# Kernel optimization log

Measured on AMD Instinct MI355X. Metric: run time of the kernel, lower is better.

The kernel has to match this reference:

```python
import jax, jax.numpy as jnp
import numpy as np

N_NODES = 100000

def gin_conv(x, edge_index, W, b):
    # PyG GINConv with eps=0: out = Linear(x + sum_{j->i} x_j)
    src, dst = edge_index[0], edge_index[1]
    agg = jax.ops.segment_sum(x[src], dst, num_segments=N_NODES)  # [N, d]
    return (x + agg) @ W + b

def setup_inputs() -> dict:
    key = jax.random.key(0)
    ks = jax.random.split(key, 8)
    x = jax.random.normal(ks[0], (N_NODES, 32), dtype=jnp.float32)
    edge_index = jax.random.randint(ks[1], (2, 1600000), 0, N_NODES, dtype=jnp.int64)
    def lin(k, fan_in, fan_out):
        kw, kb = jax.random.split(k)
        lim = 1.0 / np.sqrt(fan_in)
        W = jax.random.uniform(kw, (fan_in, fan_out), minval=-lim, maxval=lim, dtype=jnp.float32)
        b = jax.random.uniform(kb, (fan_out,), minval=-lim, maxval=lim, dtype=jnp.float32)
        return W, b
    W1, b1 = lin(ks[2], 32, 64)
    W2, b2 = lin(ks[3], 64, 64)
    W3, b3 = lin(ks[4], 64, 10)
    return {"x": x, "edge_index": edge_index,
            "W1": W1, "b1": b1, "W2": W2, "b2": b2, "W3": W3, "b3": b3}

def reference(x, edge_index, W1, b1, W2, b2, W3, b3):
    h = jax.nn.relu(gin_conv(x, edge_index, W1, b1))
    h = jax.nn.relu(gin_conv(h, edge_index, W2, b2))
    return gin_conv(h, edge_index, W3, b3)  # [N, classes] logits
```

## Files before the change

kernel.cpp:

```cpp
#include <hip/hip_runtime.h>


#define GIN_N 100000
#define NBUCKET 256
#define NB2 391
#define BSTRIDE 8192
#define EPT 16

typedef unsigned short bfu;
typedef float v2f __attribute__((ext_vector_type(2)));

__device__ __forceinline__ float bf_lo(unsigned int u) {
    return __uint_as_float(u << 16);
}
__device__ __forceinline__ float bf_hi(unsigned int u) {
    return __uint_as_float(u & 0xffff0000u);
}
__device__ __forceinline__ unsigned int f2bf(float f) {
    unsigned int u = __float_as_uint(f);
    return (u + 0x7fffu + ((u >> 16) & 1u)) >> 16;
}
__device__ __forceinline__ v2f fp8lo(unsigned u) {
    return __builtin_amdgcn_cvt_pk_f32_fp8(u, false);
}
__device__ __forceinline__ v2f fp8hi(unsigned u) {
    return __builtin_amdgcn_cvt_pk_f32_fp8(u, true);
}

template <int S>
__device__ __forceinline__ void blelloch_excl(int* a) {
#pragma unroll
    for (int d = 1; d < S; d <<= 1) {
        __syncthreads();
        int idx = (threadIdx.x + 1) * (d << 1) - 1;
        if (idx < S) a[idx] += a[idx - d];
    }
    __syncthreads();
    if (threadIdx.x == 0) a[S - 1] = 0;
#pragma unroll
    for (int d = S >> 1; d >= 1; d >>= 1) {
        __syncthreads();
        int idx = (threadIdx.x + 1) * (d << 1) - 1;
        if (idx < S) {
            int t = a[idx - d];
            a[idx - d] = a[idx];
            a[idx] += t;
        }
    }
    __syncthreads();
}

__global__ void f2q_kernel(const float* __restrict__ in,
                           unsigned* __restrict__ outq, int n8,
                           int* __restrict__ cursor) {
    int t = blockIdx.x * blockDim.x + threadIdx.x;
    if (blockIdx.x == 0) cursor[threadIdx.x] = 0;
    if (t >= n8) return;
    const float4* v = reinterpret_cast<const float4*>(in);
    float4 a = v[2 * t], b = v[2 * t + 1];
    unsigned w0 = 0, w1 = 0;
    w0 = __builtin_amdgcn_cvt_pk_fp8_f32(a.x, a.y, w0, false);
    w0 = __builtin_amdgcn_cvt_pk_fp8_f32(a.z, a.w, w0, true);
    w1 = __builtin_amdgcn_cvt_pk_fp8_f32(b.x, b.y, w1, false);
    w1 = __builtin_amdgcn_cvt_pk_fp8_f32(b.z, b.w, w1, true);
    reinterpret_cast<uint2*>(outq)[t] = make_uint2(w0, w1);
}

__global__ __launch_bounds__(256) void bucket_kernel(
        const int* __restrict__ src, const int* __restrict__ dst, int E,
        unsigned* __restrict__ bucketbuf, int* __restrict__ cursor) {
    __shared__ int h[NBUCKET];
    __shared__ int base[NBUCKET];
    int tid = threadIdx.x;
    int chunk0 = blockIdx.x * (256 * EPT);
    h[tid] = 0;
    __syncthreads();
    int myb[EPT];
    unsigned myrec[EPT];
#pragma unroll
    for (int i = 0; i < EPT; ++i) {
        int e = chunk0 + tid + i * 256;
        if (e < E) {
            int d = dst[e];
            int s = src[e];
            int b = d / NB2;
            myb[i] = b;
            myrec[i] = ((unsigned)(d - b * NB2) << 17) | (unsigned)s;
            atomicAdd(&h[b], 1);
        } else {
            myb[i] = -1;
        }
    }
    __syncthreads();
    base[tid] = atomicAdd(&cursor[tid], h[tid]);
    h[tid] = 0;
    __syncthreads();
#pragma unroll
    for (int i = 0; i < EPT; ++i) {
        int b = myb[i];
        if (b < 0) continue;
        int pos = base[b] + atomicAdd(&h[b], 1);
        if (pos < BSTRIDE) bucketbuf[(size_t)b * BSTRIDE + pos] = myrec[i];
    }
}

__global__ __launch_bounds__(256) void csr_build_kernel(
        const unsigned* __restrict__ bucketbuf,
        const int* __restrict__ cursor,
        int* __restrict__ rowptr,
        int* __restrict__ adj) {
    __shared__ int csr[BSTRIDE];
    __shared__ int cnt[512];
    __shared__ int off[512];
    __shared__ int bscan[NBUCKET];
    int b = blockIdx.x;
    int tid = threadIdx.x;
    bscan[tid] = cursor[tid];
    int mycnt = cursor[b];
    if (mycnt > BSTRIDE) mycnt = BSTRIDE;
    blelloch_excl<NBUCKET>(bscan);
    int base = bscan[b];

    const unsigned* buf = bucketbuf + (size_t)b * BSTRIDE;
    cnt[tid] = 0;
    cnt[tid + 256] = 0;
    __syncthreads();
    for (int i = tid; i < mycnt; i += 256)
        atomicAdd(&cnt[buf[i] >> 17], 1);
    __syncthreads();
    off[tid] = cnt[tid];
    off[tid + 256] = cnt[tid + 256];
    blelloch_excl<512>(off);

    int nodes0 = b * NB2;
    int nn2 = GIN_N + 1 - nodes0;
    if (nn2 > NB2) nn2 = NB2;
    for (int l = tid; l < nn2; l += 256) rowptr[nodes0 + l] = base + off[l];
    __syncthreads();

    for (int i = tid; i < mycnt; i += 256) {
        unsigned r = buf[i];
        int pos = atomicAdd(&off[r >> 17], 1);
        csr[pos] = (int)(r & 0x1FFFFu);
    }
    __syncthreads();
    for (int i = tid; i < mycnt; i += 256) adj[base + i] = csr[i];
}

__global__ __launch_bounds__(256, 8) void fused1_kernel(
        const float* __restrict__ xf,
        const unsigned* __restrict__ xq,
        const int* __restrict__ rowptr,
        const int* __restrict__ adj,
        const float* __restrict__ W,
        const float* __restrict__ b,
        bfu* __restrict__ outb,
        unsigned* __restrict__ outq) {
    constexpr int K = 32, M = 64;
    constexpr int TPN = 4, NODES = 64, TP2 = 4, MT = 16;
    constexpr int STR = K + 4;

    __shared__ unsigned Wp[K * M / 2];
    __shared__ float bs[M];
    __shared__ float tile[NODES * STR];

    for (int i = threadIdx.x; i < K * M / 2; i += 256) {
        float w0 = W[2 * i], w1 = W[2 * i + 1];
        Wp[i] = f2bf(w0) | (f2bf(w1) << 16);
    }
    if (threadIdx.x < M) bs[threadIdx.x] = b[threadIdx.x];

    int node0 = blockIdx.x * NODES;
    int tid = threadIdx.x;

    {
        int l = tid / TPN;
        int j = tid % TPN;
        int n = node0 + l;
        if (n < GIN_N) {
            int start = rowptr[n];
            int d = rowptr[n + 1] - start;
            const int* row = adj + start;
            const uint2* fq = reinterpret_cast<const uint2*>(xq);
            v2f a0, a1, a2, a3;
            {
                const float4* xv = reinterpret_cast<const float4*>(xf);
                float4 a = xv[(size_t)n * 8 + 2 * j];
                float4 c = xv[(size_t)n * 8 + 2 * j + 1];
                a0 = v2f{a.x, a.y}; a1 = v2f{a.z, a.w};
                a2 = v2f{c.x, c.y}; a3 = v2f{c.z, c.w};
            }
            int k = 0;
            for (; k + 4 <= d; k += 4) {
                uint2 v0 = fq[(size_t)row[k] * 4 + j];
                uint2 v1 = fq[(size_t)row[k + 1] * 4 + j];
                uint2 v2 = fq[(size_t)row[k + 2] * 4 + j];
                uint2 v3 = fq[(size_t)row[k + 3] * 4 + j];
                a0 += fp8lo(v0.x) + fp8lo(v1.x) + fp8lo(v2.x) + fp8lo(v3.x);
                a1 += fp8hi(v0.x) + fp8hi(v1.x) + fp8hi(v2.x) + fp8hi(v3.x);
                a2 += fp8lo(v0.y) + fp8lo(v1.y) + fp8lo(v2.y) + fp8lo(v3.y);
                a3 += fp8hi(v0.y) + fp8hi(v1.y) + fp8hi(v2.y) + fp8hi(v3.y);
            }
            for (; k < d; ++k) {
                uint2 v = fq[(size_t)row[k] * 4 + j];
                a0 += fp8lo(v.x); a1 += fp8hi(v.x);
                a2 += fp8lo(v.y); a3 += fp8hi(v.y);
            }
            float* tp = &tile[l * STR + j * 8];
            tp[0] = a0.x; tp[1] = a0.y; tp[2] = a1.x; tp[3] = a1.y;
            tp[4] = a2.x; tp[5] = a2.y; tp[6] = a3.x; tp[7] = a3.y;
        }
    }
    __syncthreads();

    {
        int l = tid / TP2;
        int sub = tid % TP2;
        int n = node0 + l;
        if (n >= GIN_N) return;
        float acc[MT];
#pragma unroll
        for (int jj = 0; jj < MT; ++jj) acc[jj] = bs[sub * MT + jj];
        const float* tp = &tile[l * STR];
#pragma unroll
        for (int k = 0; k < K; ++k) {
            float v = tp[k];
            const unsigned* wr = &Wp[k * (M / 2) + sub * (MT / 2)];
#pragma unroll
            for (int j2 = 0; j2 < MT / 2; ++j2) {
                unsigned wp = wr[j2];
                acc[2 * j2]     = fmaf(v, bf_lo(wp), acc[2 * j2]);
                acc[2 * j2 + 1] = fmaf(v, bf_hi(wp), acc[2 * j2 + 1]);
            }
        }
#pragma unroll
        for (int jj = 0; jj < MT; ++jj) acc[jj] = fmaxf(acc[jj], 0.0f);
        unsigned pb[MT / 2];
#pragma unroll
        for (int j2 = 0; j2 < MT / 2; ++j2)
            pb[j2] = f2bf(acc[2 * j2]) | (f2bf(acc[2 * j2 + 1]) << 16);
        uint4* ob = reinterpret_cast<uint4*>(outb + (size_t)n * 64 + sub * MT);
        ob[0] = make_uint4(pb[0], pb[1], pb[2], pb[3]);
        ob[1] = make_uint4(pb[4], pb[5], pb[6], pb[7]);
        unsigned q[4];
#pragma unroll
        for (int q4 = 0; q4 < 4; ++q4) {
            unsigned w = 0;
            w = __builtin_amdgcn_cvt_pk_fp8_f32(acc[4 * q4], acc[4 * q4 + 1], w, false);
            w = __builtin_amdgcn_cvt_pk_fp8_f32(acc[4 * q4 + 2], acc[4 * q4 + 3], w, true);
            q[q4] = w;
        }
        reinterpret_cast<uint4*>(outq)[(size_t)n * 4 + sub] =
            make_uint4(q[0], q[1], q[2], q[3]);
    }
}

__global__ __launch_bounds__(256, 8) void fused2_kernel(
        const bfu* __restrict__ xb,
        const unsigned* __restrict__ xq,
        const int* __restrict__ rowptr,
        const int* __restrict__ adj,
        const float* __restrict__ W,
        const float* __restrict__ b,
        bfu* __restrict__ out) {
    constexpr int K = 64, M = 64;
    constexpr int TPN = 8, NODES = 32, TP2 = 8, MT = 8;
    constexpr int STR = K + 4;

    __shared__ unsigned Wp[K * M / 2];
    __shared__ float bs[M];
    __shared__ float tile[NODES * STR];

    for (int i = threadIdx.x; i < K * M / 2; i += 256) {
        float w0 = W[2 * i], w1 = W[2 * i + 1];
        Wp[i] = f2bf(w0) | (f2bf(w1) << 16);
    }
    if (threadIdx.x < M) bs[threadIdx.x] = b[threadIdx.x];

    int node0 = blockIdx.x * NODES;
    int tid = threadIdx.x;

    {
        int l = tid / TPN;
        int j = tid % TPN;
        int n = node0 + l;
        if (n < GIN_N) {
            int start = rowptr[n];
            int d = rowptr[n + 1] - start;
            const int* row = adj + start;
            const uint2* fq = reinterpret_cast<const uint2*>(xq);
            v2f a0, a1, a2, a3;
            {
                uint4 u = reinterpret_cast<const uint4*>(xb)[(size_t)n * 8 + j];
                a0 = v2f{bf_lo(u.x), bf_hi(u.x)};
                a1 = v2f{bf_lo(u.y), bf_hi(u.y)};
                a2 = v2f{bf_lo(u.z), bf_hi(u.z)};
                a3 = v2f{bf_lo(u.w), bf_hi(u.w)};
            }
            int k = 0;
            for (; k + 4 <= d; k += 4) {
                uint2 v0 = fq[(size_t)row[k] * 8 + j];
                uint2 v1 = fq[(size_t)row[k + 1] * 8 + j];
                uint2 v2 = fq[(size_t)row[k + 2] * 8 + j];
                uint2 v3 = fq[(size_t)row[k + 3] * 8 + j];
                a0 += fp8lo(v0.x) + fp8lo(v1.x) + fp8lo(v2.x) + fp8lo(v3.x);
                a1 += fp8hi(v0.x) + fp8hi(v1.x) + fp8hi(v2.x) + fp8hi(v3.x);
                a2 += fp8lo(v0.y) + fp8lo(v1.y) + fp8lo(v2.y) + fp8lo(v3.y);
                a3 += fp8hi(v0.y) + fp8hi(v1.y) + fp8hi(v2.y) + fp8hi(v3.y);
            }
            for (; k < d; ++k) {
                uint2 v = fq[(size_t)row[k] * 8 + j];
                a0 += fp8lo(v.x); a1 += fp8hi(v.x);
                a2 += fp8lo(v.y); a3 += fp8hi(v.y);
            }
            float* tp = &tile[l * STR + j * 8];
            tp[0] = a0.x; tp[1] = a0.y; tp[2] = a1.x; tp[3] = a1.y;
            tp[4] = a2.x; tp[5] = a2.y; tp[6] = a3.x; tp[7] = a3.y;
        }
    }
    __syncthreads();

    {
        int l = tid / TP2;
        int sub = tid % TP2;
        int n = node0 + l;
        if (n >= GIN_N) return;
        float acc[MT];
#pragma unroll
        for (int jj = 0; jj < MT; ++jj) acc[jj] = bs[sub * MT + jj];
        const float* tp = &tile[l * STR];
#pragma unroll
        for (int k = 0; k < K; ++k) {
            float v = tp[k];
            const unsigned* wr = &Wp[k * (M / 2) + sub * (MT / 2)];
#pragma unroll
            for (int j2 = 0; j2 < MT / 2; ++j2) {
                unsigned wp = wr[j2];
                acc[2 * j2]     = fmaf(v, bf_lo(wp), acc[2 * j2]);
                acc[2 * j2 + 1] = fmaf(v, bf_hi(wp), acc[2 * j2 + 1]);
            }
        }
        bfu* o = out + (size_t)n * M + sub * MT;
#pragma unroll
        for (int jj = 0; jj < MT; jj += 2) {
            float r0 = fmaxf(acc[jj], 0.0f);
            float r1 = fmaxf(acc[jj + 1], 0.0f);
            unsigned p = f2bf(r0) | (f2bf(r1) << 16);
            *reinterpret_cast<unsigned*>(o + jj) = p;
        }
    }
}

__global__ __launch_bounds__(256) void mlp3_kernel(
        const bfu* __restrict__ xb,
        const float* __restrict__ W,
        bfu* __restrict__ t16) {
    constexpr int K = 64, M = 10, TPN = 2, MT = 5;
    __shared__ float Ws[K * M];
    for (int i = threadIdx.x; i < K * M; i += 256) Ws[i] = W[i];
    __syncthreads();
    int t = blockIdx.x * blockDim.x + threadIdx.x;
    int n = t / TPN;
    int sub = t % TPN;
    if (n >= GIN_N) return;
    float acc[MT] = {0, 0, 0, 0, 0};
#pragma unroll
    for (int kc = 0; kc < K / 8; ++kc) {
        uint4 u = reinterpret_cast<const uint4*>(xb)[(size_t)n * (K / 8) + kc];
        float v[8] = {bf_lo(u.x), bf_hi(u.x), bf_lo(u.y), bf_hi(u.y),
                      bf_lo(u.z), bf_hi(u.z), bf_lo(u.w), bf_hi(u.w)};
#pragma unroll
        for (int kk = 0; kk < 8; ++kk) {
            const float* wr = &Ws[(kc * 8 + kk) * M + sub * MT];
#pragma unroll
            for (int jj = 0; jj < MT; ++jj)
                acc[jj] = fmaf(v[kk], wr[jj], acc[jj]);
        }
    }
    bfu* o = t16 + (size_t)n * 16 + sub * MT;
#pragma unroll
    for (int jj = 0; jj < MT; ++jj) o[jj] = (bfu)f2bf(acc[jj]);
}

__global__ void gather_final_kernel(const unsigned* __restrict__ t8,
                                    const int* __restrict__ rowptr,
                                    const int* __restrict__ adj,
                                    const float* __restrict__ b3,
                                    float* __restrict__ out) {
    int t = blockIdx.x * blockDim.x + threadIdx.x;
    int n = t >> 3;
    int j = t & 7;
    if (n >= GIN_N || j >= 5) return;
    int start = rowptr[n];
    int d = rowptr[n + 1] - start;
    const int* row = adj + start;
    unsigned sv = t8[(size_t)n * 8 + j];
    float a0 = bf_lo(sv), a1 = bf_hi(sv);
    int k = 0;
    for (; k + 4 <= d; k += 4) {
        int r0 = row[k], r1 = row[k + 1], r2 = row[k + 2], r3 = row[k + 3];
        unsigned v0 = t8[(size_t)r0 * 8 + j];
        unsigned v1 = t8[(size_t)r1 * 8 + j];
        unsigned v2 = t8[(size_t)r2 * 8 + j];
        unsigned v3 = t8[(size_t)r3 * 8 + j];
        a0 += bf_lo(v0) + bf_lo(v1) + bf_lo(v2) + bf_lo(v3);
        a1 += bf_hi(v0) + bf_hi(v1) + bf_hi(v2) + bf_hi(v3);
    }
    for (; k < d; ++k) {
        unsigned v = t8[(size_t)row[k] * 8 + j];
        a0 += bf_lo(v); a1 += bf_hi(v);
    }
    out[(size_t)n * 10 + 2 * j] = a0 + b3[2 * j];
    out[(size_t)n * 10 + 2 * j + 1] = a1 + b3[2 * j + 1];
}

extern "C" void kernel_launch(void* const* d_in, const int* in_sizes, int n_in,
                              void* d_out, int out_size, void* d_ws, size_t ws_size,
                              hipStream_t stream) {
    const float* x  = (const float*)d_in[0];
    const int*   ei = (const int*)d_in[1];
    const float* W1 = (const float*)d_in[2];
    const float* b1 = (const float*)d_in[3];
    const float* W2 = (const float*)d_in[4];
    const float* b2 = (const float*)d_in[5];
    const float* W3 = (const float*)d_in[6];
    const float* b3 = (const float*)d_in[7];
    float* out = (float*)d_out;

    const int N = GIN_N;
    const int E = in_sizes[1] / 2;
    const int* src = ei;
    const int* dst = ei + E;

    bfu* H1b = (bfu*)d_ws;
    bfu* H2 = H1b + (size_t)N * 64;
    unsigned* H1q = (unsigned*)(H2 + (size_t)N * 64);
    unsigned* Xq = H1q + (size_t)N * 16;
    bfu* Tb = (bfu*)(Xq + (size_t)N * 8);
    int* rowptr = (int*)(Tb + (size_t)N * 16);
    int* cursor = rowptr + (N + 8);
    int* adj = cursor + 256;
    unsigned* bucketbuf = (unsigned*)(adj + (size_t)E);

    const int BLK = 256;

    f2q_kernel<<<(N * 32 / 8 + BLK - 1) / BLK, BLK, 0, stream>>>(
        x, Xq, N * 32 / 8, cursor);
    {
        int chunk = BLK * EPT;
        bucket_kernel<<<(E + chunk - 1) / chunk, BLK, 0, stream>>>(
            src, dst, E, bucketbuf, cursor);
        csr_build_kernel<<<NBUCKET, BLK, 0, stream>>>(
            bucketbuf, cursor, rowptr, adj);
    }

    fused1_kernel<<<(N + 63) / 64, BLK, 0, stream>>>(
        x, Xq, rowptr, adj, W1, b1, H1b, H1q);

    fused2_kernel<<<(N + 31) / 32, BLK, 0, stream>>>(
        H1b, H1q, rowptr, adj, W2, b2, H2);

    mlp3_kernel<<<(N * 2 + BLK - 1) / BLK, BLK, 0, stream>>>(H2, W3, Tb);
    gather_final_kernel<<<(N * 8 + BLK - 1) / BLK, BLK, 0, stream>>>(
        (const unsigned*)Tb, rowptr, adj, b3, out);
}
```

Baseline: 212.7 us.

## Fuse layer-3 linear into layer-2 kernel and merge fp8 quantize into bucketing launch

Folds the small 64x10 layer-3 projection into the layer-2 fused kernel, using an 8-lane shuffle reduction, which removes the separate mlp3 kernel and the bf16 H2 round trip. Layer 1 now writes only the fp8 copy of H1, and layer 2 reads its self term from fp8 instead of bf16, dropping a 12.8MB write and read. The x-to-fp8 conversion is merged into the bucket kernel as extra blocks, and the cursor reset becomes a memset. The trade is lower precision on the self term plus extra shared memory and registers in fused2.

```diff
diff --git a/kernel.cpp b/kernel.cpp
--- a/kernel.cpp
+++ b/kernel.cpp
@@ -50,28 +50,27 @@
     __syncthreads();
 }
 
-__global__ void f2q_kernel(const float* __restrict__ in,
-                           unsigned* __restrict__ outq, int n8,
-                           int* __restrict__ cursor) {
-    int t = blockIdx.x * blockDim.x + threadIdx.x;
-    if (blockIdx.x == 0) cursor[threadIdx.x] = 0;
-    if (t >= n8) return;
-    const float4* v = reinterpret_cast<const float4*>(in);
-    float4 a = v[2 * t], b = v[2 * t + 1];
-    unsigned w0 = 0, w1 = 0;
-    w0 = __builtin_amdgcn_cvt_pk_fp8_f32(a.x, a.y, w0, false);
-    w0 = __builtin_amdgcn_cvt_pk_fp8_f32(a.z, a.w, w0, true);
-    w1 = __builtin_amdgcn_cvt_pk_fp8_f32(b.x, b.y, w1, false);
-    w1 = __builtin_amdgcn_cvt_pk_fp8_f32(b.z, b.w, w1, true);
-    reinterpret_cast<uint2*>(outq)[t] = make_uint2(w0, w1);
-}
-
-__global__ __launch_bounds__(256) void bucket_kernel(
+__global__ __launch_bounds__(256) void build_kernel(
         const int* __restrict__ src, const int* __restrict__ dst, int E,
-        unsigned* __restrict__ bucketbuf, int* __restrict__ cursor) {
+        unsigned* __restrict__ bucketbuf, int* __restrict__ cursor,
+        const float* __restrict__ x, unsigned* __restrict__ xq, int n8,
+        int bblk) {
     __shared__ int h[NBUCKET];
     __shared__ int base[NBUCKET];
     int tid = threadIdx.x;
+    if (blockIdx.x >= bblk) {
+        int t = (blockIdx.x - bblk) * 256 + tid;
+        if (t >= n8) return;
+        const float4* v = reinterpret_cast<const float4*>(x);
+        float4 a = v[2 * t], b = v[2 * t + 1];
+        unsigned w0 = 0, w1 = 0;
+        w0 = __builtin_amdgcn_cvt_pk_fp8_f32(a.x, a.y, w0, false);
+        w0 = __builtin_amdgcn_cvt_pk_fp8_f32(a.z, a.w, w0, true);
+        w1 = __builtin_amdgcn_cvt_pk_fp8_f32(b.x, b.y, w1, false);
+        w1 = __builtin_amdgcn_cvt_pk_fp8_f32(b.z, b.w, w1, true);
+        reinterpret_cast<uint2*>(xq)[t] = make_uint2(w0, w1);
+        return;
+    }
     int chunk0 = blockIdx.x * (256 * EPT);
     h[tid] = 0;
     __syncthreads();
@@ -154,7 +153,6 @@
         const int* __restrict__ adj,
         const float* __restrict__ W,
         const float* __restrict__ b,
-        bfu* __restrict__ outb,
         unsigned* __restrict__ outq) {
     constexpr int K = 32, M = 64;
     constexpr int TPN = 4, NODES = 64, TP2 = 4, MT = 16;
@@ -235,13 +233,6 @@
         }
 #pragma unroll
         for (int jj = 0; jj < MT; ++jj) acc[jj] = fmaxf(acc[jj], 0.0f);
-        unsigned pb[MT / 2];
-#pragma unroll
-        for (int j2 = 0; j2 < MT / 2; ++j2)
-            pb[j2] = f2bf(acc[2 * j2]) | (f2bf(acc[2 * j2 + 1]) << 16);
-        uint4* ob = reinterpret_cast<uint4*>(outb + (size_t)n * 64 + sub * MT);
-        ob[0] = make_uint4(pb[0], pb[1], pb[2], pb[3]);
-        ob[1] = make_uint4(pb[4], pb[5], pb[6], pb[7]);
         unsigned q[4];
 #pragma unroll
         for (int q4 = 0; q4 < 4; ++q4) {
@@ -255,26 +246,28 @@
     }
 }
 
-__global__ __launch_bounds__(256, 8) void fused2_kernel(
-        const bfu* __restrict__ xb,
+__global__ __launch_bounds__(256, 8) void fused2t_kernel(
         const unsigned* __restrict__ xq,
         const int* __restrict__ rowptr,
         const int* __restrict__ adj,
         const float* __restrict__ W,
         const float* __restrict__ b,
-        bfu* __restrict__ out) {
+        const float* __restrict__ W3,
+        unsigned* __restrict__ tout) {
     constexpr int K = 64, M = 64;
     constexpr int TPN = 8, NODES = 32, TP2 = 8, MT = 8;
     constexpr int STR = K + 4;
 
     __shared__ unsigned Wp[K * M / 2];
     __shared__ float bs[M];
+    __shared__ float W3s[K * 10];
     __shared__ float tile[NODES * STR];
 
     for (int i = threadIdx.x; i < K * M / 2; i += 256) {
         float w0 = W[2 * i], w1 = W[2 * i + 1];
         Wp[i] = f2bf(w0) | (f2bf(w1) << 16);
     }
+    for (int i = threadIdx.x; i < K * 10; i += 256) W3s[i] = W3[i];
     if (threadIdx.x < M) bs[threadIdx.x] = b[threadIdx.x];
 
     int node0 = blockIdx.x * NODES;
@@ -291,11 +284,9 @@
             const uint2* fq = reinterpret_cast<const uint2*>(xq);
             v2f a0, a1, a2, a3;
             {
-                uint4 u = reinterpret_cast<const uint4*>(xb)[(size_t)n * 8 + j];
-                a0 = v2f{bf_lo(u.x), bf_hi(u.x)};
-                a1 = v2f{bf_lo(u.y), bf_hi(u.y)};
-                a2 = v2f{bf_lo(u.z), bf_hi(u.z)};
-                a3 = v2f{bf_lo(u.w), bf_hi(u.w)};
+                uint2 s = fq[(size_t)n * 8 + j];
+                a0 = fp8lo(s.x); a1 = fp8hi(s.x);
+                a2 = fp8lo(s.y); a3 = fp8hi(s.y);
             }
             int k = 0;
             for (; k + 4 <= d; k += 4) {
@@ -340,46 +331,37 @@
                 acc[2 * j2 + 1] = fmaf(v, bf_hi(wp), acc[2 * j2 + 1]);
             }
         }
-        bfu* o = out + (size_t)n * M + sub * MT;
-#pragma unroll
-        for (int jj = 0; jj < MT; jj += 2) {
-            float r0 = fmaxf(acc[jj], 0.0f);
-            float r1 = fmaxf(acc[jj + 1], 0.0f);
-            unsigned p = f2bf(r0) | (f2bf(r1) << 16);
-            *reinterpret_cast<unsigned*>(o + jj) = p;
-        }
-    }
-}
-
-__global__ __launch_bounds__(256) void mlp3_kernel(
-        const bfu* __restrict__ xb,
-        const float* __restrict__ W,
-        bfu* __restrict__ t16) {
-    constexpr int K = 64, M = 10, TPN = 2, MT = 5;
-    __shared__ float Ws[K * M];
-    for (int i = threadIdx.x; i < K * M; i += 256) Ws[i] = W[i];
-    __syncthreads();
-    int t = blockIdx.x * blockDim.x + threadIdx.x;
-    int n = t / TPN;
-    int sub = t % TPN;
-    if (n >= GIN_N) return;
-    float acc[MT] = {0, 0, 0, 0, 0};
-#pragma unroll
-    for (int kc = 0; kc < K / 8; ++kc) {
-        uint4 u = reinterpret_cast<const uint4*>(xb)[(size_t)n * (K / 8) + kc];
-        float v[8] = {bf_lo(u.x), bf_hi(u.x), bf_lo(u.y), bf_hi(u.y),
-                      bf_lo(u.z), bf_hi(u.z), bf_lo(u.w), bf_hi(u.w)};
-#pragma unroll
-        for (int kk = 0; kk < 8; ++kk) {
-            const float* wr = &Ws[(kc * 8 + kk) * M + sub * MT];
-#pragma unroll
-            for (int jj = 0; jj < MT; ++jj)
-                acc[jj] = fmaf(v[kk], wr[jj], acc[jj]);
-        }
-    }
-    bfu* o = t16 + (size_t)n * 16 + sub * MT;
-#pragma unroll
-    for (int jj = 0; jj < MT; ++jj) o[jj] = (bfu)f2bf(acc[jj]);
+#pragma unroll
+        for (int jj = 0; jj < MT; ++jj) acc[jj] = fmaxf(acc[jj], 0.0f);
+        float pt[10];
+#pragma unroll
+        for (int jj = 0; jj < 10; ++jj) pt[jj] = 0.0f;
+#pragma unroll
+        for (int kk = 0; kk < MT; ++kk) {
+            float v = acc[kk];
+            const float* wr = &W3s[(sub * MT + kk) * 10];
+#pragma unroll
+            for (int jj = 0; jj < 10; ++jj) pt[jj] = fmaf(v, wr[jj], pt[jj]);
+        }
+#pragma unroll
+        for (int jj = 0; jj < 10; ++jj) {
+            float v = pt[jj];
+            v += __shfl_xor(v, 1, 64);
+            v += __shfl_xor(v, 2, 64);
+            v += __shfl_xor(v, 4, 64);
+            pt[jj] = v;
+        }
+        if (sub == 0) {
+            unsigned p[8];
+#pragma unroll
+            for (int j2 = 0; j2 < 5; ++j2)
+                p[j2] = f2bf(pt[2 * j2]) | (f2bf(pt[2 * j2 + 1]) << 16);
+            p[5] = 0; p[6] = 0; p[7] = 0;
+            uint4* o = reinterpret_cast<uint4*>(tout) + (size_t)n * 2;
+            o[0] = make_uint4(p[0], p[1], p[2], p[3]);
+            o[1] = make_uint4(p[4], p[5], p[6], p[7]);
+        }
+    }
 }
 
 __global__ void gather_final_kernel(const unsigned* __restrict__ t8,
@@ -432,35 +414,33 @@
     const int* src = ei;
     const int* dst = ei + E;
 
-    bfu* H1b = (bfu*)d_ws;
-    bfu* H2 = H1b + (size_t)N * 64;
-    unsigned* H1q = (unsigned*)(H2 + (size_t)N * 64);
-    unsigned* Xq = H1q + (size_t)N * 16;
-    bfu* Tb = (bfu*)(Xq + (size_t)N * 8);
-    int* rowptr = (int*)(Tb + (size_t)N * 16);
+    unsigned* Xq = (unsigned*)d_ws;
+    unsigned* H1q = Xq + (size_t)N * 8;
+    unsigned* Tb = H1q + (size_t)N * 16;
+    int* rowptr = (int*)(Tb + (size_t)N * 8);
     int* cursor = rowptr + (N + 8);
     int* adj = cursor + 256;
     unsigned* bucketbuf = (unsigned*)(adj + (size_t)E);
 
     const int BLK = 256;
 
-    f2q_kernel<<<(N * 32 / 8 + BLK - 1) / BLK, BLK, 0, stream>>>(
-        x, Xq, N * 32 / 8, cursor);
+    hipMemsetAsync(cursor, 0, 256 * sizeof(int), stream);
     {
-        int chunk = BLK * EPT;
-        bucket_kernel<<<(E + chunk - 1) / chunk, BLK, 0, stream>>>(
-            src, dst, E, bucketbuf, cursor);
+        int n8 = N * 32 / 8;
+        int bblk = (E + BLK * EPT - 1) / (BLK * EPT);
+        int xblk = (n8 + BLK - 1) / BLK;
+        build_kernel<<<bblk + xblk, BLK, 0, stream>>>(
+            src, dst, E, bucketbuf, cursor, x, Xq, n8, bblk);
         csr_build_kernel<<<NBUCKET, BLK, 0, stream>>>(
             bucketbuf, cursor, rowptr, adj);
     }
 
     fused1_kernel<<<(N + 63) / 64, BLK, 0, stream>>>(
-        x, Xq, rowptr, adj, W1, b1, H1b, H1q);
-
-    fused2_kernel<<<(N + 31) / 32, BLK, 0, stream>>>(
-        H1b, H1q, rowptr, adj, W2, b2, H2);
-
-    mlp3_kernel<<<(N * 2 + BLK - 1) / BLK, BLK, 0, stream>>>(H2, W3, Tb);
+        x, Xq, rowptr, adj, W1, b1, H1q);
+
+    fused2t_kernel<<<(N + 31) / 32, BLK, 0, stream>>>(
+        H1q, rowptr, adj, W2, b2, W3, Tb);
+
     gather_final_kernel<<<(N * 8 + BLK - 1) / BLK, BLK, 0, stream>>>(
-        (const unsigned*)Tb, rowptr, adj, b3, out);
-}
+        Tb, rowptr, adj, b3, out);
+}
```

Result: no change. 208.8 us (-1.8%).
